# Kernel optimization log

Measured on AMD Instinct MI355X. Metric: run time of the kernel, lower is better.

The kernel has to match this reference:

```python
import jax, jax.numpy as jnp
import numpy as np

B, K, D = 4, 2048, 512   # batch, time window (self._K), d_model
H, Q, V = 8, 64, 64      # heads, per-head query dim, per-head value dim


def setup_inputs() -> dict:
    key = jax.random.key(0)
    ks = jax.random.split(key, 10)
    s = 0.05
    return {
        "query": jax.random.normal(ks[0], (B, K, D), jnp.float32),
        "key":   jax.random.normal(ks[1], (B, K, D), jnp.float32),
        "value": jax.random.normal(ks[2], (B, K, D), jnp.float32),
        # stacked per-head Linear params (torch Linear: y = x W^T + b -> store as [h, D, out])
        "W_q": jax.random.normal(ks[3], (H, D, Q), jnp.float32) * s,
        "b_q": jax.random.normal(ks[4], (H, Q), jnp.float32) * s,
        "W_k": jax.random.normal(ks[5], (H, D, Q), jnp.float32) * s,
        "b_k": jax.random.normal(ks[6], (H, Q), jnp.float32) * s,
        "W_v": jax.random.normal(ks[7], (H, D, V), jnp.float32) * s,
        "b_v": jax.random.normal(ks[8], (H, V), jnp.float32) * s,
        "W_o": jax.random.normal(ks[9], (H * V, D), jnp.float32) * s,
        "b_o": jnp.zeros((D,), jnp.float32),
    }


def reference(query, key, value, W_q, b_q, W_k, b_k, W_v, b_v, W_o, b_o):
    # per-head projections, batched over heads: [B, H, K, Q/V]
    q = jnp.einsum("bkd,hdq->bhkq", query, W_q) + b_q[None, :, None, :]
    k = jnp.einsum("bkd,hdq->bhkq", key,   W_k) + b_k[None, :, None, :]
    v = jnp.einsum("bkd,hdv->bhkv", value, W_v) + b_v[None, :, None, :]
    # NOTE: original divides by sqrt(self._K) (time window), NOT sqrt(d_k)
    scores = jnp.einsum("bhkq,bhlq->bhkl", q, k) / np.sqrt(K).astype(np.float32)
    # mask == 'subsequent': causal triu mask above the diagonal
    causal = jnp.triu(jnp.ones((K, K), bool), k=1)
    scores = jnp.where(causal[None, None], -jnp.inf, scores)
    attn = jax.nn.softmax(scores, axis=-1)
    heads = jnp.einsum("bhkl,bhlv->bhkv", attn, v)          # [B, H, K, V]
    concat = heads.transpose(0, 2, 1, 3).reshape(B, K, H * V)  # concat along last dim
    return concat @ W_o + b_o
```

## Files before the change

kernel.cpp:

```cpp
#include <hip/hip_runtime.h>
#include <hip/hip_bf16.h>

typedef __attribute__((ext_vector_type(8))) short bf16x8;
typedef __attribute__((ext_vector_type(4))) float f32x4;

#define SEQ 2048
#define DM  512
#define NH  8
#define DH  64
#define QSCALE 0.031879360f

__device__ __forceinline__ unsigned short f2bf(float f) {
  unsigned int u = __float_as_uint(f);
  unsigned int r = 0x7FFFu + ((u >> 16) & 1u);
  return (unsigned short)((u + r) >> 16);
}

__device__ __forceinline__ void cvt8f(const float4& v0, const float4& v1,
                                      unsigned short* __restrict__ o) {
  o[0] = f2bf(v0.x); o[1] = f2bf(v0.y); o[2] = f2bf(v0.z); o[3] = f2bf(v0.w);
  o[4] = f2bf(v1.x); o[5] = f2bf(v1.y); o[6] = f2bf(v1.z); o[7] = f2bf(v1.w);
}

__device__ __forceinline__ void load8f(const float* __restrict__ s,
                                       unsigned short* __restrict__ o) {
  float4 v0 = *(const float4*)s;
  float4 v1 = *(const float4*)(s + 4);
  cvt8f(v0, v1, o);
}

__global__ __launch_bounds__(256) void weight_prep(const float* __restrict__ Wq,
                                                   const float* __restrict__ Wk,
                                                   const float* __restrict__ Wv,
                                                   const float* __restrict__ Wo,
                                                   unsigned short* __restrict__ Wqt,
                                                   unsigned short* __restrict__ Wkt,
                                                   unsigned short* __restrict__ Wvt,
                                                   unsigned short* __restrict__ Wot) {
  const int which = blockIdx.x >> 6, wi = blockIdx.x & 63;
  const float* src;
  unsigned short* dst;
  int R, C, r0, c0;
  if (which < 3) {
    const float* W = (which == 0) ? Wq : (which == 1) ? Wk : Wv;
    unsigned short* D = (which == 0) ? Wqt : (which == 1) ? Wkt : Wvt;
    int h = wi >> 3;
    src = W + (size_t)h * 512 * 64;
    dst = D + (size_t)h * 64 * 512;
    R = 512; C = 64; r0 = (wi & 7) * 64; c0 = 0;
  } else {
    src = Wo; dst = Wot;
    R = 512; C = 512; r0 = (wi >> 3) * 64; c0 = (wi & 7) * 64;
  }
  __shared__ __align__(16) unsigned short T[64][72];
  const int tid = threadIdx.x;
#pragma unroll
  for (int i = 0; i < 2; ++i) {
    int c = tid + 256 * i;
    int lr = c >> 3, lc = (c & 7) * 8;
    __align__(16) unsigned short tmp[8];
    load8f(src + (size_t)(r0 + lr) * C + c0 + lc, tmp);
    *(uint4*)&T[lr][lc] = *(const uint4*)tmp;
  }
  __syncthreads();
#pragma unroll
  for (int i = 0; i < 2; ++i) {
    int c = tid + 256 * i;
    int orow = c >> 3, och = (c & 7) * 8;
    __align__(16) unsigned short tmp[8];
#pragma unroll
    for (int j = 0; j < 8; ++j) tmp[j] = T[och + j][orow];
    *(uint4*)(dst + (size_t)(c0 + orow) * R + r0 + och) = *(uint4*)tmp;
  }
}

__global__ __launch_bounds__(256, 2) void proj128(const float* __restrict__ q,
                                                  const float* __restrict__ k,
                                                  const float* __restrict__ v,
                                                  const unsigned short* __restrict__ Wqt,
                                                  const unsigned short* __restrict__ Wkt,
                                                  const unsigned short* __restrict__ Wvt,
                                                  const float* __restrict__ bq,
                                                  const float* __restrict__ bk,
                                                  const float* __restrict__ bv,
                                                  unsigned short* __restrict__ Qp,
                                                  unsigned short* __restrict__ Kp,
                                                  unsigned short* __restrict__ Vpt) {
  const int which = blockIdx.z;
  const float* X = (which == 0) ? q : (which == 1) ? k : v;
  const unsigned short* Wt = (which == 0) ? Wqt : (which == 1) ? Wkt : Wvt;
  const float* bias = (which == 0) ? bq : (which == 1) ? bk : bv;
  unsigned short* out = (which == 0) ? Qp : (which == 1) ? Kp : Vpt;
  const float ps = (which == 0) ? QSCALE : 1.0f;

  const int m0 = blockIdx.x * 128;
  const int n0 = blockIdx.y * 128;
  __shared__ __align__(16) unsigned short As[2][128][72], Bs[2][128][72];
  const int tid  = threadIdx.x;
  const int wave = tid >> 6, lane = tid & 63;
  const int l15  = lane & 15, quad = lane >> 4;
  const int rb = (wave >> 1) * 64, cb = (wave & 1) * 64;

  f32x4 acc[4][4];
#pragma unroll
  for (int i = 0; i < 4; ++i)
#pragma unroll
    for (int f = 0; f < 4; ++f) acc[i][f] = (f32x4){0.f, 0.f, 0.f, 0.f};

  float4 af[4][2];
  uint4 bst[4];

#define P_LOAD(k0_) do {                                                        \
    _Pragma("unroll")                                                           \
    for (int i_ = 0; i_ < 4; ++i_) {                                            \
      int c_ = tid + 256 * i_;                                                  \
      int lr_ = c_ >> 3, lc_ = (c_ & 7) * 8;                                    \
      const float* xp_ = X + (size_t)(m0 + lr_) * DM + (k0_) + lc_;             \
      af[i_][0] = *(const float4*)xp_;                                          \
      af[i_][1] = *(const float4*)(xp_ + 4);                                    \
      bst[i_] = *(const uint4*)(Wt + (size_t)(n0 + lr_) * DM + (k0_) + lc_);    \
    } } while (0)

#define P_WRITE(bi_) do {                                                       \
    _Pragma("unroll")                                                           \
    for (int i_ = 0; i_ < 4; ++i_) {                                            \
      int c_ = tid + 256 * i_;                                                  \
      int lr_ = c_ >> 3, lc_ = (c_ & 7) * 8;                                    \
      __align__(16) unsigned short t_[8];                                       \
      cvt8f(af[i_][0], af[i_][1], t_);                                          \
      *(uint4*)&As[bi_][lr_][lc_] = *(const uint4*)t_;                          \
      *(uint4*)&Bs[bi_][lr_][lc_] = bst[i_];                                    \
    } } while (0)

  P_LOAD(0);
  P_WRITE(0);
  P_LOAD(64);
  __syncthreads();

#pragma unroll 1
  for (int k0i = 0; k0i < 8; ++k0i) {
    const int cur = k0i & 1;
    if (k0i < 7) P_WRITE(cur ^ 1);
    if (k0i < 6) P_LOAD((k0i + 2) * 64);
#pragma unroll
    for (int kc = 0; kc < 2; ++kc) {
      bf16x8 av[4], bv4[4];
#pragma unroll
      for (int i = 0; i < 4; ++i) av[i]  = *(const bf16x8*)&As[cur][rb + 16 * i + l15][kc * 32 + quad * 8];
#pragma unroll
      for (int f = 0; f < 4; ++f) bv4[f] = *(const bf16x8*)&Bs[cur][cb + 16 * f + l15][kc * 32 + quad * 8];
#pragma unroll
      for (int i = 0; i < 4; ++i)
#pragma unroll
        for (int f = 0; f < 4; ++f)
          acc[i][f] = __builtin_amdgcn_mfma_f32_16x16x32_bf16(av[i], bv4[f], acc[i][f], 0, 0, 0);
    }
    __syncthreads();
  }
#undef P_LOAD
#undef P_WRITE

  if (which < 2) {
#pragma unroll
    for (int i = 0; i < 4; ++i)
#pragma unroll
      for (int f = 0; f < 4; ++f)
#pragma unroll
        for (int r = 0; r < 4; ++r) {
          int m = m0 + rb + 16 * i + quad * 4 + r;
          int col = n0 + cb + 16 * f + l15;
          int head = col >> 6, o = col & 63;
          int b = m >> 11, s = m & (SEQ - 1);
          float val = (acc[i][f][r] + bias[col]) * ps;
          out[(((size_t)(b * NH + head) * SEQ + s) << 6) + o] = f2bf(val);
        }
  } else {
    __syncthreads();
    unsigned short* T = &As[0][0][0] + wave * 4608;
#pragma unroll
    for (int i = 0; i < 4; ++i)
#pragma unroll
      for (int f = 0; f < 4; ++f)
#pragma unroll
        for (int r = 0; r < 4; ++r) {
          int lrow = 16 * i + quad * 4 + r;
          int lcol = 16 * f + l15;
          int col = n0 + cb + 16 * f + l15;
          T[lcol * 72 + lrow] = f2bf(acc[i][f][r] + bias[col]);
        }
    const int mbase = m0 + rb;
    const int b = mbase >> 11, sbase = mbase & (SEQ - 1);
    const int head = (n0 + cb) >> 6;
    unsigned short* dstb = out + ((size_t)(b * NH + head) * DH) * SEQ + sbase;
#pragma unroll
    for (int j = 0; j < 8; ++j) {
      int dh = (lane >> 3) + j * 8;
      int sc = (lane & 7) * 8;
      *(uint4*)(dstb + (size_t)dh * SEQ + sc) = *(const uint4*)&T[dh * 72 + sc];
    }
  }
}

__global__ __launch_bounds__(512, 4) void attn_kernel(const unsigned short* __restrict__ Qp,
                                                      const unsigned short* __restrict__ Kp,
                                                      const unsigned short* __restrict__ Vpt,
                                                      unsigned short* __restrict__ concat) {
  const int bh = blockIdx.x;
  const int ip = blockIdx.y;
  const int b = bh >> 3, h = bh & 7;
  const int qa = ip, qb = 31 - ip;
  __shared__ __align__(16) unsigned short Ks[2][64][72], Vts[2][64][72], Ps[128][76];
  const int tid  = threadIdx.x;
  const int wave = tid >> 6, lane = tid & 63;
  const int l15  = lane & 15, quad = lane >> 4;
  const int w4   = wave & 3;
  const bool isB = wave < 4;
  const int qt   = isB ? qb : qa;
  const unsigned short* Qb = Qp  + (size_t)bh * SEQ * DH;
  const unsigned short* Kb = Kp  + (size_t)bh * SEQ * DH;
  const unsigned short* Vb = Vpt + (size_t)bh * DH * SEQ;

  bf16x8 aq[2];
#pragma unroll
  for (int kc = 0; kc < 2; ++kc)
    aq[kc] = *(const bf16x8*)(Qb + (size_t)(qt * 64 + 16 * w4 + l15) * DH + kc * 32 + quad * 8);

  float l_lane[4];
  f32x4 Of[4];
#pragma unroll
  for (int r = 0; r < 4; ++r) l_lane[r] = 0.f;
#pragma unroll
  for (int f = 0; f < 4; ++f) Of[f] = (f32x4){0.f, 0.f, 0.f, 0.f};

  const int sr = tid >> 3, sc = (tid & 7) * 8;
  uint4 kst, vst;

#define STAGE_LOAD(lt_) do {                                                   \
    kst = *(const uint4*)(Kb + (size_t)((lt_) * 64 + sr) * DH + sc);           \
    vst = *(const uint4*)(Vb + (size_t)sr * SEQ + (lt_) * 64 + sc);            \
  } while (0)

#define STAGE_WRITE(bi_) do {                                                  \
    *(uint4*)&Ks[bi_][sr][sc]  = kst;                                          \
    *(uint4*)&Vts[bi_][sr][sc] = vst;                                          \
  } while (0)

  STAGE_LOAD(0);
  STAGE_WRITE(0);
  STAGE_LOAD(1);
  __syncthreads();

#pragma unroll 1
  for (int lt = 0; lt <= qb; ++lt) {
    const int cur = lt & 1;
    if (lt < qb) STAGE_WRITE(cur ^ 1);
    if (lt + 2 <= qb) STAGE_LOAD(lt + 2);

    const bool act = isB || (lt <= qa);
    if (act) {
      const int l0 = lt * 64;
      f32x4 S[4];
#pragma unroll
      for (int f = 0; f < 4; ++f) S[f] = (f32x4){0.f, 0.f, 0.f, 0.f};
#pragma unroll
      for (int kc = 0; kc < 2; ++kc) {
#pragma unroll
        for (int f = 0; f < 4; ++f) {
          bf16x8 bk = *(const bf16x8*)&Ks[cur][16 * f + l15][kc * 32 + quad * 8];
          S[f] = __builtin_amdgcn_mfma_f32_16x16x32_bf16(aq[kc], bk, S[f], 0, 0, 0);
        }
      }
      if (lt == qt) {
        const int mrow = qt * 64 + 16 * w4 + quad * 4;
#pragma unroll
        for (int f = 0; f < 4; ++f)
#pragma unroll
          for (int r = 0; r < 4; ++r)
            if (l0 + 16 * f + l15 > mrow + r) S[f][r] = -1e30f;
      }
#pragma unroll
      for (int f = 0; f < 4; ++f)
#pragma unroll
        for (int r = 0; r < 4; ++r) {
          float p = __builtin_amdgcn_exp2f(S[f][r]);
          l_lane[r] += p;
          Ps[wave * 16 + quad * 4 + r][16 * f + l15] = f2bf(p);
        }
#pragma unroll
      for (int kc = 0; kc < 2; ++kc) {
        bf16x8 ap = *(const bf16x8*)&Ps[wave * 16 + l15][kc * 32 + quad * 8];
#pragma unroll
        for (int f = 0; f < 4; ++f) {
          bf16x8 bvv = *(const bf16x8*)&Vts[cur][16 * f + l15][kc * 32 + quad * 8];
          Of[f] = __builtin_amdgcn_mfma_f32_16x16x32_bf16(ap, bvv, Of[f], 0, 0, 0);
        }
      }
    }
    __syncthreads();
  }
#undef STAGE_LOAD
#undef STAGE_WRITE

#pragma unroll
  for (int d = 1; d < 16; d <<= 1)
#pragma unroll
    for (int r = 0; r < 4; ++r) l_lane[r] += __shfl_xor(l_lane[r], d);

#pragma unroll
  for (int f = 0; f < 4; ++f)
#pragma unroll
    for (int r = 0; r < 4; ++r) {
      const int row = qt * 64 + 16 * w4 + quad * 4 + r;
      const int col = h * DH + 16 * f + l15;
      concat[(size_t)(b * SEQ + row) * DM + col] = f2bf(Of[f][r] / l_lane[r]);
    }
}

__global__ __launch_bounds__(256, 2) void gemm_out(const unsigned short* __restrict__ A,
                                                   const unsigned short* __restrict__ Bt,
                                                   const float* __restrict__ bias,
                                                   float* __restrict__ out) {
  const int m0 = blockIdx.x * 64;
  const int nbase = blockIdx.y * 128;
  __shared__ __align__(16) unsigned short Bs[2][64][72];
  const int tid  = threadIdx.x;
  const int wave = tid >> 6, lane = tid & 63;
  const int l15  = lane & 15, quad = lane >> 4;

  bf16x8 afr[16];
  const unsigned short* arow = A + (size_t)(m0 + 16 * wave + l15) * DM;
#pragma unroll
  for (int k0i = 0; k0i < 8; ++k0i)
#pragma unroll
    for (int kc = 0; kc < 2; ++kc)
      afr[k0i * 2 + kc] = *(const bf16x8*)(arow + k0i * 64 + kc * 32 + quad * 8);

  uint4 bst0, bst1;
  const int br = tid >> 3, bc = (tid & 7) * 8;

#define G_LOAD(s_) do {                                                          \
    const int n0_ = nbase + ((s_) >> 3) * 64, k0_ = ((s_) & 7) * 64;             \
    bst0 = *(const uint4*)(Bt + (size_t)(n0_ + br) * DM + k0_ + bc);             \
    bst1 = *(const uint4*)(Bt + (size_t)(n0_ + br + 32) * DM + k0_ + bc);        \
  } while (0)

#define G_WRITE(bi_) do {                                                        \
    *(uint4*)&Bs[bi_][br][bc]      = bst0;                                       \
    *(uint4*)&Bs[bi_][br + 32][bc] = bst1;                                       \
  } while (0)

  f32x4 acc[2][4];
#pragma unroll
  for (int nh = 0; nh < 2; ++nh)
#pragma unroll
    for (int f = 0; f < 4; ++f) acc[nh][f] = (f32x4){0.f, 0.f, 0.f, 0.f};

  G_LOAD(0);
  G_WRITE(0);
  G_LOAD(1);
  __syncthreads();

#pragma unroll
  for (int s = 0; s < 16; ++s) {
    const int cur = s & 1;
    if (s < 15) G_WRITE(cur ^ 1);
    if (s < 14) G_LOAD(s + 2);
    const int nh = s >> 3, k0i = s & 7;
#pragma unroll
    for (int kc = 0; kc < 2; ++kc)
#pragma unroll
      for (int f = 0; f < 4; ++f) {
        bf16x8 bfv = *(const bf16x8*)&Bs[cur][16 * f + l15][kc * 32 + quad * 8];
        acc[nh][f] = __builtin_amdgcn_mfma_f32_16x16x32_bf16(afr[k0i * 2 + kc], bfv, acc[nh][f], 0, 0, 0);
      }
    __syncthreads();
  }
#undef G_LOAD
#undef G_WRITE

#pragma unroll
  for (int nh = 0; nh < 2; ++nh)
#pragma unroll
    for (int f = 0; f < 4; ++f)
#pragma unroll
      for (int r = 0; r < 4; ++r) {
        int row = 16 * wave + quad * 4 + r;
        int col = nbase + nh * 64 + 16 * f + l15;
        out[(size_t)(m0 + row) * DM + col] = acc[nh][f][r] + bias[col];
      }
}

extern "C" void kernel_launch(void* const* d_in, const int* in_sizes, int n_in,
                              void* d_out, int out_size, void* d_ws, size_t ws_size,
                              hipStream_t stream) {
  const float* query = (const float*)d_in[0];
  const float* key   = (const float*)d_in[1];
  const float* value = (const float*)d_in[2];
  const float* W_q   = (const float*)d_in[3];
  const float* b_q   = (const float*)d_in[4];
  const float* W_k   = (const float*)d_in[5];
  const float* b_k   = (const float*)d_in[6];
  const float* W_v   = (const float*)d_in[7];
  const float* b_v   = (const float*)d_in[8];
  const float* W_o   = (const float*)d_in[9];
  const float* b_o   = (const float*)d_in[10];
  float* out = (float*)d_out;

  char* ws = (char*)d_ws;
  unsigned short* Wqt    = (unsigned short*)(ws + 0);
  unsigned short* Wkt    = (unsigned short*)(ws + 524288);
  unsigned short* Wvt    = (unsigned short*)(ws + 1048576);
  unsigned short* Wot    = (unsigned short*)(ws + 1572864);
  unsigned short* Qp     = (unsigned short*)(ws + 2097152);
  unsigned short* Kp     = (unsigned short*)(ws + 10485760);
  unsigned short* Vpt    = (unsigned short*)(ws + 18874368);
  unsigned short* concat = (unsigned short*)(ws + 27262976);

  weight_prep<<<dim3(256), 256, 0, stream>>>(W_q, W_k, W_v, W_o, Wqt, Wkt, Wvt, Wot);

  proj128<<<dim3(64, 4, 3), 256, 0, stream>>>(query, key, value, Wqt, Wkt, Wvt,
                                              b_q, b_k, b_v, Qp, Kp, Vpt);

  attn_kernel<<<dim3(32, 16), 512, 0, stream>>>(Qp, Kp, Vpt, concat);

  gemm_out<<<dim3(128, 4), 256, 0, stream>>>(concat, Wot, b_o, out);
}
```

Measured before the change: 206.8 us.

## Pre-convert activations to bf16 in prep kernel and single-buffer projection GEMM

Adds a conversion pass to the weight-prep kernel that turns the fp32 query/key/value activations into bf16 in a workspace buffer. The projection GEMM then loads bf16 directly, so the fp32-to-bf16 conversion leaves its inner loop and each tile load moves half the bytes. The GEMM's register-prefetch double buffering is replaced with a simple single-buffered sync/load/sync loop, halving shared memory so the launch bound can allow 4 blocks per CU. The cost is an extra full read of fp32 activations plus a bf16 write and re-read through global memory, and the loss of load/compute overlap inside the GEMM.

```diff
diff --git a/kernel.cpp b/kernel.cpp
--- a/kernel.cpp
+++ b/kernel.cpp
@@ -33,10 +33,30 @@
                                                    const float* __restrict__ Wk,
                                                    const float* __restrict__ Wv,
                                                    const float* __restrict__ Wo,
+                                                   const float* __restrict__ q,
+                                                   const float* __restrict__ k,
+                                                   const float* __restrict__ v,
                                                    unsigned short* __restrict__ Wqt,
                                                    unsigned short* __restrict__ Wkt,
                                                    unsigned short* __restrict__ Wvt,
-                                                   unsigned short* __restrict__ Wot) {
+                                                   unsigned short* __restrict__ Wot,
+                                                   unsigned short* __restrict__ Xb) {
+  const int tid = threadIdx.x;
+  if (blockIdx.x >= 256) {
+    const int wi = blockIdx.x - 256;
+    const float* src = (wi < 128) ? q : (wi < 256) ? k : v;
+    const size_t off = (size_t)(wi & 127) * 32768;
+    const float* s = src + off;
+    unsigned short* d = Xb + (size_t)(wi >> 7) * (4u * SEQ * DM) + off;
+#pragma unroll
+    for (int i = 0; i < 16; ++i) {
+      const size_t idx = (size_t)(tid + 256 * i) * 8;
+      __align__(16) unsigned short t[8];
+      load8f(s + idx, t);
+      *(uint4*)(d + idx) = *(const uint4*)t;
+    }
+    return;
+  }
   const int which = blockIdx.x >> 6, wi = blockIdx.x & 63;
   const float* src;
   unsigned short* dst;
@@ -53,7 +73,6 @@
     R = 512; C = 512; r0 = (wi >> 3) * 64; c0 = (wi & 7) * 64;
   }
   __shared__ __align__(16) unsigned short T[64][72];
-  const int tid = threadIdx.x;
 #pragma unroll
   for (int i = 0; i < 2; ++i) {
     int c = tid + 256 * i;
@@ -74,9 +93,7 @@
   }
 }
 
-__global__ __launch_bounds__(256, 2) void proj128(const float* __restrict__ q,
-                                                  const float* __restrict__ k,
-                                                  const float* __restrict__ v,
+__global__ __launch_bounds__(256, 4) void proj128(const unsigned short* __restrict__ Xb,
                                                   const unsigned short* __restrict__ Wqt,
                                                   const unsigned short* __restrict__ Wkt,
                                                   const unsigned short* __restrict__ Wvt,
@@ -87,7 +104,7 @@
                                                   unsigned short* __restrict__ Kp,
                                                   unsigned short* __restrict__ Vpt) {
   const int which = blockIdx.z;
-  const float* X = (which == 0) ? q : (which == 1) ? k : v;
+  const unsigned short* X = Xb + (size_t)which * (4u * SEQ * DM);
   const unsigned short* Wt = (which == 0) ? Wqt : (which == 1) ? Wkt : Wvt;
   const float* bias = (which == 0) ? bq : (which == 1) ? bk : bv;
   unsigned short* out = (which == 0) ? Qp : (which == 1) ? Kp : Vpt;
@@ -95,7 +112,9 @@
 
   const int m0 = blockIdx.x * 128;
   const int n0 = blockIdx.y * 128;
-  __shared__ __align__(16) unsigned short As[2][128][72], Bs[2][128][72];
+  __shared__ __align__(16) unsigned short smem[2][128][72];
+  unsigned short (*As)[72] = smem[0];
+  unsigned short (*Bs)[72] = smem[1];
   const int tid  = threadIdx.x;
   const int wave = tid >> 6, lane = tid & 63;
   const int l15  = lane & 15, quad = lane >> 4;
@@ -107,58 +126,30 @@
 #pragma unroll
     for (int f = 0; f < 4; ++f) acc[i][f] = (f32x4){0.f, 0.f, 0.f, 0.f};
 
-  float4 af[4][2];
-  uint4 bst[4];
-
-#define P_LOAD(k0_) do {                                                        \
-    _Pragma("unroll")                                                           \
-    for (int i_ = 0; i_ < 4; ++i_) {                                            \
-      int c_ = tid + 256 * i_;                                                  \
-      int lr_ = c_ >> 3, lc_ = (c_ & 7) * 8;                                    \
-      const float* xp_ = X + (size_t)(m0 + lr_) * DM + (k0_) + lc_;             \
-      af[i_][0] = *(const float4*)xp_;                                          \
-      af[i_][1] = *(const float4*)(xp_ + 4);                                    \
-      bst[i_] = *(const uint4*)(Wt + (size_t)(n0 + lr_) * DM + (k0_) + lc_);    \
-    } } while (0)
-
-#define P_WRITE(bi_) do {                                                       \
-    _Pragma("unroll")                                                           \
-    for (int i_ = 0; i_ < 4; ++i_) {                                            \
-      int c_ = tid + 256 * i_;                                                  \
-      int lr_ = c_ >> 3, lc_ = (c_ & 7) * 8;                                    \
-      __align__(16) unsigned short t_[8];                                       \
-      cvt8f(af[i_][0], af[i_][1], t_);                                          \
-      *(uint4*)&As[bi_][lr_][lc_] = *(const uint4*)t_;                          \
-      *(uint4*)&Bs[bi_][lr_][lc_] = bst[i_];                                    \
-    } } while (0)
-
-  P_LOAD(0);
-  P_WRITE(0);
-  P_LOAD(64);
-  __syncthreads();
-
-#pragma unroll 1
-  for (int k0i = 0; k0i < 8; ++k0i) {
-    const int cur = k0i & 1;
-    if (k0i < 7) P_WRITE(cur ^ 1);
-    if (k0i < 6) P_LOAD((k0i + 2) * 64);
+  for (int k0 = 0; k0 < DM; k0 += 64) {
+    __syncthreads();
+#pragma unroll
+    for (int i = 0; i < 4; ++i) {
+      int c = tid + 256 * i;
+      int lr = c >> 3, lc = (c & 7) * 8;
+      *(uint4*)&As[lr][lc] = *(const uint4*)(X  + (size_t)(m0 + lr) * DM + k0 + lc);
+      *(uint4*)&Bs[lr][lc] = *(const uint4*)(Wt + (size_t)(n0 + lr) * DM + k0 + lc);
+    }
+    __syncthreads();
 #pragma unroll
     for (int kc = 0; kc < 2; ++kc) {
       bf16x8 av[4], bv4[4];
 #pragma unroll
-      for (int i = 0; i < 4; ++i) av[i]  = *(const bf16x8*)&As[cur][rb + 16 * i + l15][kc * 32 + quad * 8];
-#pragma unroll
-      for (int f = 0; f < 4; ++f) bv4[f] = *(const bf16x8*)&Bs[cur][cb + 16 * f + l15][kc * 32 + quad * 8];
+      for (int i = 0; i < 4; ++i) av[i]  = *(const bf16x8*)&As[rb + 16 * i + l15][kc * 32 + quad * 8];
+#pragma unroll
+      for (int f = 0; f < 4; ++f) bv4[f] = *(const bf16x8*)&Bs[cb + 16 * f + l15][kc * 32 + quad * 8];
 #pragma unroll
       for (int i = 0; i < 4; ++i)
 #pragma unroll
         for (int f = 0; f < 4; ++f)
           acc[i][f] = __builtin_amdgcn_mfma_f32_16x16x32_bf16(av[i], bv4[f], acc[i][f], 0, 0, 0);
     }
-    __syncthreads();
-  }
-#undef P_LOAD
-#undef P_WRITE
+  }
 
   if (which < 2) {
 #pragma unroll
@@ -176,7 +167,7 @@
         }
   } else {
     __syncthreads();
-    unsigned short* T = &As[0][0][0] + wave * 4608;
+    unsigned short* T = &smem[0][0][0] + wave * 4608;
 #pragma unroll
     for (int i = 0; i < 4; ++i)
 #pragma unroll
@@ -415,10 +406,12 @@
   unsigned short* Kp     = (unsigned short*)(ws + 10485760);
   unsigned short* Vpt    = (unsigned short*)(ws + 18874368);
   unsigned short* concat = (unsigned short*)(ws + 27262976);
-
-  weight_prep<<<dim3(256), 256, 0, stream>>>(W_q, W_k, W_v, W_o, Wqt, Wkt, Wvt, Wot);
-
-  proj128<<<dim3(64, 4, 3), 256, 0, stream>>>(query, key, value, Wqt, Wkt, Wvt,
+  unsigned short* Xb     = (unsigned short*)(ws + 35651584);
+
+  weight_prep<<<dim3(640), 256, 0, stream>>>(W_q, W_k, W_v, W_o, query, key, value,
+                                             Wqt, Wkt, Wvt, Wot, Xb);
+
+  proj128<<<dim3(64, 4, 3), 256, 0, stream>>>(Xb, Wqt, Wkt, Wvt,
                                               b_q, b_k, b_v, Qp, Kp, Vpt);
 
   attn_kernel<<<dim3(32, 16), 512, 0, stream>>>(Qp, Kp, Vpt, concat);
```

Measured after the change: 184.0 us. 1.12x faster.
